# Kernel tuning notes

Measured on AMD Instinct MI355X. Metric: run time of the kernel, lower is better.

## Reference

```python
import jax, jax.numpy as jnp
import numpy as np

D = 256           # input_dim
PROCESS_STEP = 4
N_SUPPORT = 512
BATCH = 32768


def setup_inputs() -> dict:
    key = jax.random.key(0)
    ks = jax.random.split(key, 8)
    H = 2 * D  # LSTMCell hidden size
    scale = 0.05
    return {
        "support_mean": jax.random.normal(ks[0], (N_SUPPORT, D), jnp.float32),
        "support_var": jax.random.uniform(ks[1], (N_SUPPORT, D), jnp.float32),
        "query_mean": jax.random.normal(ks[2], (BATCH, D), jnp.float32),
        "query_var": jax.random.uniform(ks[3], (BATCH, D), jnp.float32),
        # LSTMCell(D, 2D) parameters (PyTorch layout: [4*H, in] / [4*H, H])
        "W_ih": jax.random.normal(ks[4], (4 * H, D), jnp.float32) * scale,
        "W_hh": jax.random.normal(ks[5], (4 * H, H), jnp.float32) * scale,
        "b_ih": jax.random.normal(ks[6], (4 * H,), jnp.float32) * scale,
        "b_hh": jax.random.normal(ks[7], (4 * H,), jnp.float32) * scale,
    }


def _lstm_cell(x, h, c, W_ih, W_hh, b_ih, b_hh):
    # gates: [B, 4H], PyTorch gate order: input, forget, cell(g), output
    gates = x @ W_ih.T + b_ih + h @ W_hh.T + b_hh
    i, f, g, o = jnp.split(gates, 4, axis=1)
    i = jax.nn.sigmoid(i)
    f = jax.nn.sigmoid(f)
    g = jnp.tanh(g)
    o = jax.nn.sigmoid(o)
    c_new = f * c + i * g
    h_new = o * jnp.tanh(c_new)
    return h_new, c_new


def reference(support_mean, support_var, query_mean, query_var,
              W_ih, W_hh, b_ih, b_hh):
    # support_var / query_var are unused by the original forward.
    B = query_mean.shape[0]
    H = 2 * D
    h_r = jnp.zeros((B, H), query_mean.dtype)
    c = jnp.zeros((B, H), query_mean.dtype)
    h = query_mean  # placeholder; overwritten in first step
    for _ in range(PROCESS_STEP):
        h_r_, c = _lstm_cell(query_mean, h_r, c, W_ih, W_hh, b_ih, b_hh)
        h = query_mean + h_r_[:, :D]                       # [B, D]
        attn = jax.nn.softmax(h @ support_mean.T, axis=1)   # [B, S]
        r = attn @ support_mean                              # [B, D]
        h_r = jnp.concatenate((h, r), axis=1)                # [B, 2D]
    matching_scores = jnp.squeeze(h @ support_mean.T)        # [B, S]
    return matching_scores
```

## Files before the change

### kernel.cpp

```cpp
#include <hip/hip_runtime.h>

typedef unsigned int uint;
typedef unsigned short ushort;
typedef __attribute__((ext_vector_type(8))) short bhalf8;
typedef __attribute__((ext_vector_type(4))) float floatx4;

#define D_IN 256
#define NUNIT 256
#define GN 1024
#define NSUP 512
#define BATCH_N 32768
#define LDA_A 768

__device__ __forceinline__ ushort f2b(float f){
  union { float f; uint u; } x; x.f = f;
  uint r = (x.u + 0x7fffu + ((x.u >> 16) & 1u)) >> 16;
  return (ushort)r;
}
__device__ __forceinline__ float b2f(ushort u){
  union { uint u; float f; } x; x.u = ((uint)u) << 16;
  return x.f;
}
__device__ __forceinline__ float sigmf(float x){ return 1.0f / (1.0f + __expf(-x)); }
__device__ __forceinline__ float tanhfast(float x){ return 1.0f - 2.0f / (1.0f + __expf(2.0f * x)); }

__device__ __forceinline__ void stage_rows8(
    ushort* lds_base, const ushort* __restrict__ g, int ld,
    long grow0, int lrow0, int k0, int lane)
{
  const int rsub = lane >> 3;
  const int oct  = (lane & 7) ^ rsub;
  const ushort* gp = g + (grow0 + lrow0 + rsub) * ld + k0 + (oct << 3);
  ushort* lp = lds_base + lrow0 * 64;
  __builtin_amdgcn_global_load_lds(
      (const __attribute__((address_space(1))) void*)gp,
      (__attribute__((address_space(3))) void*)lp, 16, 0, 0);
}

__device__ __forceinline__ void stage_swz4(
    ushort* lds, const ushort* __restrict__ g, int ld, int row0, int k0,
    int wave, int lane)
{
  #pragma unroll
  for (int q = 0; q < 4; q++)
    stage_rows8(lds, g, ld, row0, wave * 32 + q * 8, k0, lane);
}

__device__ __forceinline__ void stage_swz8(
    ushort* lds, const ushort* __restrict__ g, int ld, int row0, int k0,
    int wave, int lane)
{
  #pragma unroll
  for (int q = 0; q < 2; q++)
    stage_rows8(lds, g, ld, row0, wave * 16 + q * 8, k0, lane);
}

__device__ __forceinline__ bhalf8 frag_ld(const ushort* lds, int R, int O, int sx)
{
  return *reinterpret_cast<const bhalf8*>(&lds[R * 64 + (((O ^ sx) & 7) << 3)]);
}

__device__ __forceinline__ bhalf8 frag_ld512(const ushort* lds, int R, int g, int O, int sx)
{
  return *reinterpret_cast<const bhalf8*>(&lds[R * 512 + g * 64 + (((O ^ sx) & 7) << 3)]);
}

__global__ __launch_bounds__(512) void gemm_gq_fused(
    const ushort* __restrict__ Qb,
    const ushort* __restrict__ Wq,
    const float4* __restrict__ biasp,
    uint2* __restrict__ Gq,
    float* __restrict__ cbuf,
    const float* __restrict__ query,
    ushort* __restrict__ Hhi,
    ushort* __restrict__ Hlo)
{
  __shared__ ushort SM[2][8192];

  const int tid  = threadIdx.x;
  const int lane = tid & 63;
  const int wave = tid >> 6;
  const int wrow = (wave >> 1) * 32;
  const int wcol = (wave & 1) * 64;
  const int wg = (blockIdx.x & 7) * (gridDim.x >> 3) + (blockIdx.x >> 3);
  const int bm = wg >> 3;
  const int bn = wg & 7;
  const int rowA0 = bm * 128;
  const int colB0 = bn * 128;

  floatx4 acc[2][4];
  #pragma unroll
  for (int m = 0; m < 2; m++)
    #pragma unroll
    for (int n = 0; n < 4; n++)
      acc[m][n] = (floatx4){0.f, 0.f, 0.f, 0.f};

  const int lr = lane & 15;
  const int lg = lane >> 4;
  const int sx = lane & 7;

  for (int k0 = 0; k0 < 256; k0 += 64) {
    stage_swz8(SM[0], Qb, 256, rowA0, k0, wave, lane);
    stage_swz8(SM[1], Wq, 256, colB0, k0, wave, lane);
    __syncthreads();
    #pragma unroll
    for (int ks = 0; ks < 2; ks++) {
      bhalf8 af[2], bfr[4];
      #pragma unroll
      for (int m = 0; m < 2; m++)
        af[m] = frag_ld(SM[0], wrow + m * 16 + lr, ks * 4 + lg, sx);
      #pragma unroll
      for (int n = 0; n < 4; n++)
        bfr[n] = frag_ld(SM[1], wcol + n * 16 + lr, ks * 4 + lg, sx);
      #pragma unroll
      for (int m = 0; m < 2; m++)
        #pragma unroll
        for (int n = 0; n < 4; n++)
          acc[m][n] = __builtin_amdgcn_mfma_f32_16x16x32_bf16(af[m], bfr[n], acc[m][n], 0, 0, 0);
    }
    __syncthreads();
  }

  ushort* ehi = (ushort*)SM[0];
  ushort* elo = ehi + 128 * 32;
  float*  ec  = (float*)SM[1];

  const int u_loc = (wave & 1) * 16 + lr;
  const int u     = bn * 32 + u_loc;
  const float4 b4 = biasp[u];
  #pragma unroll
  for (int m = 0; m < 2; m++) {
    #pragma unroll
    for (int rr = 0; rr < 4; rr++) {
      const int  rloc = wrow + m * 16 + lg * 4 + rr;
      const long row  = rowA0 + rloc;
      float pi = acc[m][0][rr] + b4.x;
      float pf = acc[m][1][rr] + b4.y;
      float pg = acc[m][2][rr] + b4.z;
      float po = acc[m][3][rr] + b4.w;
      uint2 pk;
      pk.x = (uint)f2b(pi) | ((uint)f2b(pf) << 16);
      pk.y = (uint)f2b(pg) | ((uint)f2b(po) << 16);
      Gq[row * NUNIT + u] = pk;
      float cn = sigmf(pi) * tanhfast(pg);
      ec[rloc * 32 + u_loc] = cn;
      float h = query[row * D_IN + u] + sigmf(po) * tanhfast(cn);
      ushort hh = f2b(h);
      ehi[rloc * 32 + u_loc] = hh;
      elo[rloc * 32 + u_loc] = f2b(h - b2f(hh));
    }
  }
  __syncthreads();
  const int u0 = bn * 32;
  {
    int row = tid >> 2, part = tid & 3;
    *(uint4*)(Hhi + (long)(rowA0 + row) * LDA_A + u0 + part * 8) = ((const uint4*)ehi)[tid];
    *(uint4*)(Hlo + (long)(rowA0 + row) * D_IN + u0 + part * 8) = ((const uint4*)elo)[tid];
  }
  #pragma unroll
  for (int i = tid; i < 1024; i += 512) {
    int row = i >> 3, part = i & 7;
    *(uint4*)(cbuf + (long)(rowA0 + row) * NUNIT + u0 + part * 4) = ((const uint4*)ec)[i];
  }
}

__global__ __launch_bounds__(512) void gemm_gates_fused(
    const ushort* __restrict__ A,
    const ushort* __restrict__ W,
    const uint2* __restrict__ Gq,
    float* __restrict__ cbuf,
    const float* __restrict__ query,
    ushort* __restrict__ Hhi,
    ushort* __restrict__ Hlo)
{
  __shared__ ushort SM[2][2][8192];

  const int tid  = threadIdx.x;
  const int lane = tid & 63;
  const int wave = tid >> 6;
  const int wrow = (wave >> 1) * 32;
  const int wcol = (wave & 1) * 64;
  const int wg = (blockIdx.x & 7) * (gridDim.x >> 3) + (blockIdx.x >> 3);
  const int bm = wg >> 3;
  const int bn = wg & 7;
  const int rowA0 = bm * 128;
  const int colB0 = bn * 128;

  floatx4 acc[2][4];
  #pragma unroll
  for (int m = 0; m < 2; m++)
    #pragma unroll
    for (int n = 0; n < 4; n++)
      acc[m][n] = (floatx4){0.f, 0.f, 0.f, 0.f};

  const int lr = lane & 15;
  const int lg = lane >> 4;
  const int sx = lane & 7;

  stage_swz8(SM[0][0], A, LDA_A, rowA0, 0, wave, lane);
  stage_swz8(SM[0][1], W, 512,   colB0, 0, wave, lane);
  __syncthreads();

  for (int t = 0; t < 8; t++) {
    const int cur = t & 1;
    if (t + 1 < 8) {
      stage_swz8(SM[cur ^ 1][0], A, LDA_A, rowA0, (t + 1) * 64, wave, lane);
      stage_swz8(SM[cur ^ 1][1], W, 512,   colB0, (t + 1) * 64, wave, lane);
    }
    const ushort* As = SM[cur][0];
    const ushort* Bs = SM[cur][1];
    #pragma unroll
    for (int ks = 0; ks < 2; ks++) {
      bhalf8 af[2], bfr[4];
      #pragma unroll
      for (int m = 0; m < 2; m++)
        af[m] = frag_ld(As, wrow + m * 16 + lr, ks * 4 + lg, sx);
      #pragma unroll
      for (int n = 0; n < 4; n++)
        bfr[n] = frag_ld(Bs, wcol + n * 16 + lr, ks * 4 + lg, sx);
      #pragma unroll
      for (int m = 0; m < 2; m++)
        #pragma unroll
        for (int n = 0; n < 4; n++)
          acc[m][n] = __builtin_amdgcn_mfma_f32_16x16x32_bf16(af[m], bfr[n], acc[m][n], 0, 0, 0);
    }
    __syncthreads();
  }

  ushort* ehi = (ushort*)SM[0][0];
  ushort* elo = ehi + 128 * 32;
  float*  ec  = (float*)SM[0][1];

  const int u_loc = (wave & 1) * 16 + lr;
  const int u     = bn * 32 + u_loc;
  #pragma unroll
  for (int m = 0; m < 2; m++) {
    #pragma unroll
    for (int rr = 0; rr < 4; rr++) {
      const int  rloc = wrow + m * 16 + lg * 4 + rr;
      const long row  = rowA0 + rloc;
      uint2 pk = Gq[row * NUNIT + u];
      float pi = acc[m][0][rr] + b2f((ushort)(pk.x & 0xffff));
      float pf = acc[m][1][rr] + b2f((ushort)(pk.x >> 16));
      float pg = acc[m][2][rr] + b2f((ushort)(pk.y & 0xffff));
      float po = acc[m][3][rr] + b2f((ushort)(pk.y >> 16));
      float cn = sigmf(pf) * cbuf[row * NUNIT + u] + sigmf(pi) * tanhfast(pg);
      ec[rloc * 32 + u_loc] = cn;
      float h = query[row * D_IN + u] + sigmf(po) * tanhfast(cn);
      ushort hh = f2b(h);
      ehi[rloc * 32 + u_loc] = hh;
      elo[rloc * 32 + u_loc] = f2b(h - b2f(hh));
    }
  }
  __syncthreads();
  const int u0 = bn * 32;
  {
    int row = tid >> 2, part = tid & 3;
    *(uint4*)(Hhi + (long)(rowA0 + row) * LDA_A + u0 + part * 8) = ((const uint4*)ehi)[tid];
    *(uint4*)(Hlo + (long)(rowA0 + row) * D_IN + u0 + part * 8) = ((const uint4*)elo)[tid];
  }
  #pragma unroll
  for (int i = tid; i < 1024; i += 512) {
    int row = i >> 3, part = i & 7;
    *(uint4*)(cbuf + (long)(rowA0 + row) * NUNIT + u0 + part * 4) = ((const uint4*)ec)[i];
  }
}

__global__ __launch_bounds__(256) void gemm_scores(
    const ushort* __restrict__ Ahi,
    const ushort* __restrict__ Alo,
    const ushort* __restrict__ Bhi, const ushort* __restrict__ Blo,
    float* __restrict__ C)
{
  __shared__ ushort AsH[128 * 64];
  __shared__ ushort AsL[128 * 64];
  __shared__ ushort BsH[128 * 64];
  __shared__ ushort BsL[128 * 64];

  const int tid  = threadIdx.x;
  const int lane = tid & 63;
  const int wave = tid >> 6;
  const int wr = (wave >> 1) * 64;
  const int wc = (wave & 1) * 64;
  const int wg = (blockIdx.x & 7) * (gridDim.x >> 3) + (blockIdx.x >> 3);
  const int bm = wg >> 2;
  const int bn = wg & 3;
  const int rowA0 = bm * 128;
  const int rowB0 = bn * 128;

  floatx4 acc[4][4];
  #pragma unroll
  for (int m = 0; m < 4; m++)
    #pragma unroll
    for (int n = 0; n < 4; n++)
      acc[m][n] = (floatx4){0.f, 0.f, 0.f, 0.f};

  const int lr = lane & 15;
  const int lg = lane >> 4;
  const int sx = lane & 7;

  for (int k0 = 0; k0 < D_IN; k0 += 64) {
    stage_swz4(AsH, Ahi, LDA_A, rowA0, k0, wave, lane);
    stage_swz4(AsL, Alo, D_IN,  rowA0, k0, wave, lane);
    stage_swz4(BsH, Bhi, D_IN,  rowB0, k0, wave, lane);
    stage_swz4(BsL, Blo, D_IN,  rowB0, k0, wave, lane);
    __syncthreads();
    #pragma unroll
    for (int ks = 0; ks < 2; ks++) {
      bhalf8 afh[4], afl[4], bfh[4], bfl[4];
      #pragma unroll
      for (int m = 0; m < 4; m++) {
        afh[m] = frag_ld(AsH, wr + m * 16 + lr, ks * 4 + lg, sx);
        afl[m] = frag_ld(AsL, wr + m * 16 + lr, ks * 4 + lg, sx);
      }
      #pragma unroll
      for (int n = 0; n < 4; n++) {
        bfh[n] = frag_ld(BsH, wc + n * 16 + lr, ks * 4 + lg, sx);
        bfl[n] = frag_ld(BsL, wc + n * 16 + lr, ks * 4 + lg, sx);
      }
      #pragma unroll
      for (int m = 0; m < 4; m++)
        #pragma unroll
        for (int n = 0; n < 4; n++) {
          acc[m][n] = __builtin_amdgcn_mfma_f32_16x16x32_bf16(afl[m], bfh[n], acc[m][n], 0, 0, 0);
          acc[m][n] = __builtin_amdgcn_mfma_f32_16x16x32_bf16(afh[m], bfl[n], acc[m][n], 0, 0, 0);
          acc[m][n] = __builtin_amdgcn_mfma_f32_16x16x32_bf16(afh[m], bfh[n], acc[m][n], 0, 0, 0);
        }
    }
    __syncthreads();
  }

  #pragma unroll
  for (int m = 0; m < 4; m++)
    #pragma unroll
    for (int n = 0; n < 4; n++)
      #pragma unroll
      for (int r = 0; r < 4; r++) {
        int row = rowA0 + wr + m * 16 + lg * 4 + r;
        int col = rowB0 + wc + n * 16 + lr;
        C[(long)row * NSUP + col] = acc[m][n][r];
      }
}

__global__ __launch_bounds__(512) void k_sspv(
    const ushort* __restrict__ Ahi,
    const ushort* __restrict__ Alo,
    const ushort* __restrict__ Shi,
    const ushort* __restrict__ Slo,
    const ushort* __restrict__ STb,
    ushort* __restrict__ Cv)
{
  __shared__ ushort SMEM[65536];
  ushort* Areg = SMEM;
  ushort* Breg = SMEM + 32768;

  const int tid  = threadIdx.x;
  const int lane = tid & 63;
  const int wave = tid >> 6;
  const int wg = (blockIdx.x & 7) * (gridDim.x >> 3) + (blockIdx.x >> 3);
  const long rowA0 = (long)wg * 64;

  const int lr = lane & 15;
  const int lg = lane >> 4;
  const int sx = lane & 7;

  {
    const ushort* asrc = (wave < 4) ? Ahi : Alo;
    const int ald = (wave < 4) ? LDA_A : D_IN;
    ushort* adst = Areg + (wave >> 2) * 16384 + (wave & 3) * 4096;
    const int ak0 = (wave & 3) * 64;
    #pragma unroll
    for (int q = 0; q < 8; q++)
      stage_rows8(adst, asrc, ald, rowA0, q * 8, ak0, lane);
  }
  #pragma unroll
  for (int q = 0; q < 8; q++)
    stage_rows8(Breg, Shi, D_IN, 0, wave * 64 + q * 8, 0, lane);
  __syncthreads();

  floatx4 acc[4][4];
  #pragma unroll
  for (int m = 0; m < 4; m++)
    #pragma unroll
    for (int n = 0; n < 4; n++)
      acc[m][n] = (floatx4){0.f, 0.f, 0.f, 0.f};

  for (int kc = 0; kc < 4; kc++) {
    const ushort* Ah = Areg + kc * 4096;
    const ushort* Al = Areg + 16384 + kc * 4096;
    #pragma unroll
    for (int ks = 0; ks < 2; ks++) {
      bhalf8 afh[4], afl[4], bfh[4];
      #pragma unroll
      for (int m = 0; m < 4; m++) {
        afh[m] = frag_ld(Ah, m * 16 + lr, ks * 4 + lg, sx);
        afl[m] = frag_ld(Al, m * 16 + lr, ks * 4 + lg, sx);
      }
      #pragma unroll
      for (int n = 0; n < 4; n++)
        bfh[n] = frag_ld(Breg, wave * 64 + n * 16 + lr, ks * 4 + lg, sx);
      #pragma unroll
      for (int m = 0; m < 4; m++)
        #pragma unroll
        for (int n = 0; n < 4; n++) {
          acc[m][n] = __builtin_amdgcn_mfma_f32_16x16x32_bf16(afl[m], bfh[n], acc[m][n], 0, 0, 0);
          acc[m][n] = __builtin_amdgcn_mfma_f32_16x16x32_bf16(afh[m], bfh[n], acc[m][n], 0, 0, 0);
        }
    }
    __syncthreads();
    #pragma unroll
    for (int q = 0; q < 8; q++)
      stage_rows8(Breg, Slo, D_IN, 0, wave * 64 + q * 8, kc * 64, lane);
    __syncthreads();
    #pragma unroll
    for (int ks = 0; ks < 2; ks++) {
      bhalf8 afh[4], bfl[4];
      #pragma unroll
      for (int m = 0; m < 4; m++)
        afh[m] = frag_ld(Ah, m * 16 + lr, ks * 4 + lg, sx);
      #pragma unroll
      for (int n = 0; n < 4; n++)
        bfl[n] = frag_ld(Breg, wave * 64 + n * 16 + lr, ks * 4 + lg, sx);
      #pragma unroll
      for (int m = 0; m < 4; m++)
        #pragma unroll
        for (int n = 0; n < 4; n++)
          acc[m][n] = __builtin_amdgcn_mfma_f32_16x16x32_bf16(afh[m], bfl[n], acc[m][n], 0, 0, 0);
    }
    __syncthreads();
    if (kc < 3) {
      #pragma unroll
      for (int q = 0; q < 8; q++)
        stage_rows8(Breg, Shi, D_IN, 0, wave * 64 + q * 8, (kc + 1) * 64, lane);
      __syncthreads();
    }
  }

  float*  scf = (float*)Breg;
  ushort* Ps  = Areg;
  const int po  = (lane >> 1) & 7;
  const int ph4 = (lane & 1) * 4;
  const int pg0 = lane >> 4;

  #pragma unroll
  for (int half = 0; half < 2; half++) {
    #pragma unroll
    for (int mm = 0; mm < 2; mm++) {
      const int m = half * 2 + mm;
      #pragma unroll
      for (int n = 0; n < 4; n++)
        #pragma unroll
        for (int r = 0; r < 4; r++)
          scf[(mm * 16 + lg * 4 + r) * 512 + wave * 64 + n * 16 + lr] = acc[m][n][r];
    }
    __syncthreads();
    #pragma unroll
    for (int j = 0; j < 4; j++) {
      const int rl = wave * 4 + j;
      const int r  = half * 32 + rl;
      const float4* sp = reinterpret_cast<const float4*>(scf + rl * 512);
      float4 v0 = sp[lane];
      float4 v1 = sp[64 + lane];
      float m = fmaxf(fmaxf(fmaxf(v0.x, v0.y), fmaxf(v0.z, v0.w)),
                      fmaxf(fmaxf(v1.x, v1.y), fmaxf(v1.z, v1.w)));
      #pragma unroll
      for (int off = 32; off >= 1; off >>= 1) m = fmaxf(m, __shfl_xor(m, off));
      float e0 = __expf(v0.x - m), e1 = __expf(v0.y - m), e2 = __expf(v0.z - m), e3 = __expf(v0.w - m);
      float e4 = __expf(v1.x - m), e5 = __expf(v1.y - m), e6 = __expf(v1.z - m), e7 = __expf(v1.w - m);
      float s = e0 + e1 + e2 + e3 + e4 + e5 + e6 + e7;
      #pragma unroll
      for (int off = 32; off >= 1; off >>= 1) s += __shfl_xor(s, off);
      float inv = 1.0f / s;
      uint2 p0, p1;
      p0.x = (uint)f2b(e0 * inv) | ((uint)f2b(e1 * inv) << 16);
      p0.y = (uint)f2b(e2 * inv) | ((uint)f2b(e3 * inv) << 16);
      p1.x = (uint)f2b(e4 * inv) | ((uint)f2b(e5 * inv) << 16);
      p1.y = (uint)f2b(e6 * inv) | ((uint)f2b(e7 * inv) << 16);
      const int os = ((po ^ (r & 7)) << 3) + ph4;
      *(uint2*)&Ps[r * 512 + (pg0    ) * 64 + os] = p0;
      *(uint2*)&Ps[r * 512 + (pg0 + 4) * 64 + os] = p1;
    }
    __syncthreads();
  }

  floatx4 pacc[4][2];
  #pragma unroll
  for (int m = 0; m < 4; m++)
    #pragma unroll
    for (int n = 0; n < 2; n++)
      pacc[m][n] = (floatx4){0.f, 0.f, 0.f, 0.f};

  ushort* Bpv = Breg;
  for (int kc = 0; kc < 8; kc++) {
    #pragma unroll
    for (int q = 0; q < 4; q++)
      stage_rows8(Bpv, STb, NSUP, 0, wave * 32 + q * 8, kc * 64, lane);
    __syncthreads();
    #pragma unroll
    for (int ks = 0; ks < 2; ks++) {
      bhalf8 af[4], bfr[2];
      #pragma unroll
      for (int m = 0; m < 4; m++)
        af[m] = frag_ld512(Ps, m * 16 + lr, kc, ks * 4 + lg, sx);
      #pragma unroll
      for (int n = 0; n < 2; n++)
        bfr[n] = frag_ld(Bpv, wave * 32 + n * 16 + lr, ks * 4 + lg, sx);
      #pragma unroll
      for (int m = 0; m < 4; m++)
        #pragma unroll
        for (int n = 0; n < 2; n++)
          pacc[m][n] = __builtin_amdgcn_mfma_f32_16x16x32_bf16(af[m], bfr[n], pacc[m][n], 0, 0, 0);
    }
    __syncthreads();
  }

  ushort* elr = Breg + 16384;
  #pragma unroll
  for (int m = 0; m < 4; m++)
    #pragma unroll
    for (int n = 0; n < 2; n++)
      #pragma unroll
      for (int r = 0; r < 4; r++)
        elr[(m * 16 + lg * 4 + r) * 256 + wave * 32 + n * 16 + lr] = f2b(pacc[m][n][r]);
  __syncthreads();
  #pragma unroll
  for (int i = tid; i < 2048; i += 512) {
    int row = i >> 5, part = i & 31;
    *(uint4*)(Cv + (rowA0 + row) * LDA_A + part * 8) = ((const uint4*)elr)[i];
  }
}

__global__ __launch_bounds__(256) void k_build(
    const float* __restrict__ Wih, const float* __restrict__ Whh,
    const float* __restrict__ bih, const float* __restrict__ bhh,
    const float* __restrict__ S,
    ushort* __restrict__ We, ushort* __restrict__ Wo, ushort* __restrict__ Wq,
    float4* __restrict__ biasp,
    ushort* __restrict__ Shi, ushort* __restrict__ Slo,
    ushort* __restrict__ STb)
{
  int t = blockIdx.x * 256 + threadIdx.x;
  if (t < GN * 512) {
    int c = t >> 9, k = t & 511;
    int unit = (c >> 6) * 16 + (c & 15);
    int gate = (c >> 4) & 3;
    long srow = (long)(gate * 512 + unit);
    We[(long)c * 512 + k] = f2b(Whh[srow * 512 + k]);
    int ko = (k < 256) ? (256 + k) : (k - 256);
    Wo[(long)c * 512 + k] = f2b(Whh[srow * 512 + ko]);
    if (k < 256) Wq[(long)c * 256 + k] = f2b(Wih[srow * 256 + k]);
  }
  if (t < NUNIT) {
    biasp[t] = make_float4(bih[t] + bhh[t],
                           bih[512 + t] + bhh[512 + t],
                           bih[1024 + t] + bhh[1024 + t],
                           bih[1536 + t] + bhh[1536 + t]);
  }
  if (t < NSUP * D_IN) {
    float v = S[t];
    ushort hv = f2b(v);
    Shi[t] = hv;
    Slo[t] = f2b(v - b2f(hv));
    int s = t >> 8, d = t & 255;
    STb[(long)d * NSUP + s] = hv;
  }
}

__global__ __launch_bounds__(256) void k_initq(
    const float* __restrict__ query, ushort* __restrict__ Qb)
{
  long t = (long)blockIdx.x * 256 + threadIdx.x;
  Qb[t] = f2b(query[t]);
}

extern "C" void kernel_launch(void* const* d_in, const int* in_sizes, int n_in,
                              void* d_out, int out_size, void* d_ws, size_t ws_size,
                              hipStream_t stream)
{
  const float* support_mean = (const float*)d_in[0];
  const float* query_mean   = (const float*)d_in[2];
  const float* W_ih = (const float*)d_in[4];
  const float* W_hh = (const float*)d_in[5];
  const float* b_ih = (const float*)d_in[6];
  const float* b_hh = (const float*)d_in[7];
  float* out = (float*)d_out;

  char* ws = (char*)d_ws;
  size_t off = 0;
  auto alloc = [&](size_t bytes) {
    void* p = ws + off;
    off += (bytes + 255) & ~(size_t)255;
    return p;
  };
  ushort* Abuf  = (ushort*)alloc((size_t)BATCH_N * LDA_A * 2);
  ushort* Qb    = (ushort*)alloc((size_t)BATCH_N * D_IN * 2);
  ushort* We    = (ushort*)alloc((size_t)GN * 512 * 2);
  ushort* Wo    = (ushort*)alloc((size_t)GN * 512 * 2);
  ushort* Wq    = (ushort*)alloc((size_t)GN * 256 * 2);
  float4* biasp = (float4*)alloc((size_t)NUNIT * 16);
  ushort* Shi   = (ushort*)alloc((size_t)NSUP * D_IN * 2);
  ushort* Slo   = (ushort*)alloc((size_t)NSUP * D_IN * 2);
  ushort* STb   = (ushort*)alloc((size_t)D_IN * NSUP * 2);
  float*  cbuf  = (float*) alloc((size_t)BATCH_N * NUNIT * 4);
  ushort* Hlo   = (ushort*)alloc((size_t)BATCH_N * D_IN * 2);
  uint2*  Gq    = (uint2*) alloc((size_t)BATCH_N * NUNIT * 8);
  if (off > ws_size) return;

  hipLaunchKernelGGL(k_build, dim3((GN * 512) / 256), dim3(256), 0, stream,
                     W_ih, W_hh, b_ih, b_hh, support_mean,
                     We, Wo, Wq, biasp, Shi, Slo, STb);
  hipLaunchKernelGGL(k_initq, dim3((BATCH_N * D_IN) / 256), dim3(256), 0, stream,
                     query_mean, Qb);

  hipLaunchKernelGGL(gemm_gq_fused,
                     dim3((BATCH_N / 128) * (GN / 128)), dim3(512), 0, stream,
                     Qb, Wq, biasp, Gq, cbuf, query_mean, Abuf + 0, Hlo);

  for (int s = 0; s < 3; s++) {
    const int hoff = (s & 1) * 512;
    hipLaunchKernelGGL(k_sspv, dim3(BATCH_N / 64), dim3(512), 0, stream,
                       Abuf + hoff, Hlo, Shi, Slo, STb, Abuf + 256);
    const int aoff = ((s + 1) == 2) ? 256 : 0;
    const ushort* Wnext = ((s + 1) == 2) ? Wo : We;
    hipLaunchKernelGGL(gemm_gates_fused,
                       dim3((BATCH_N / 128) * (GN / 128)), dim3(512), 0, stream,
                       Abuf + aoff, Wnext, Gq, cbuf, query_mean,
                       Abuf + ((s + 1) & 1) * 512, Hlo);
  }
  hipLaunchKernelGGL(gemm_scores,
                     dim3((BATCH_N / 128) * (NSUP / 128)), dim3(256), 0, stream,
                     Abuf + 512, Hlo, Shi, Slo, out);
}
```

Measured before the change: 469.0 us.

## Halve k_sspv row tile to 32 and shrink LDS to 64KB for occupancy

The attention kernel k_sspv now processes 32 query rows per workgroup instead of 64 and stages the support matrix in 32-wide K chunks with a new 4-way swizzle. LDS use drops from 128KB to 64KB, which could allow two workgroups per CU and doubles the grid size. In exchange, every workgroup still streams the full support matrices, so support-side global traffic and barrier count per row roughly double.

```diff
diff --git a/kernel.cpp b/kernel.cpp
--- a/kernel.cpp
+++ b/kernel.cpp
@@ -37,6 +37,19 @@
       (__attribute__((address_space(3))) void*)lp, 16, 0, 0);
 }
 
+__device__ __forceinline__ void stage_rows16_32(
+    ushort* lds_base, const ushort* __restrict__ g, int ld,
+    long grow0, int lrow0, int k0, int lane)
+{
+  const int rsub = lane >> 2;
+  const int oct  = (lane & 3) ^ ((rsub >> 1) & 3);
+  const ushort* gp = g + (grow0 + lrow0 + rsub) * ld + k0 + (oct << 3);
+  ushort* lp = lds_base + lrow0 * 32;
+  __builtin_amdgcn_global_load_lds(
+      (const __attribute__((address_space(1))) void*)gp,
+      (__attribute__((address_space(3))) void*)lp, 16, 0, 0);
+}
+
 __device__ __forceinline__ void stage_swz4(
     ushort* lds, const ushort* __restrict__ g, int ld, int row0, int k0,
     int wave, int lane)
@@ -58,6 +71,11 @@
 __device__ __forceinline__ bhalf8 frag_ld(const ushort* lds, int R, int O, int sx)
 {
   return *reinterpret_cast<const bhalf8*>(&lds[R * 64 + (((O ^ sx) & 7) << 3)]);
+}
+
+__device__ __forceinline__ bhalf8 frag32_ld(const ushort* lds, int R, int O)
+{
+  return *reinterpret_cast<const bhalf8*>(&lds[R * 32 + (((O ^ (R >> 1)) & 3) << 3)]);
 }
 
 __device__ __forceinline__ bhalf8 frag_ld512(const ushort* lds, int R, int g, int O, int sx)
@@ -350,15 +368,14 @@
     const ushort* __restrict__ STb,
     ushort* __restrict__ Cv)
 {
-  __shared__ ushort SMEM[65536];
-  ushort* Areg = SMEM;
-  ushort* Breg = SMEM + 32768;
+  __shared__ ushort SMEM[32768];
+  ushort* Sbuf = SMEM + 16384;
 
   const int tid  = threadIdx.x;
   const int lane = tid & 63;
   const int wave = tid >> 6;
   const int wg = (blockIdx.x & 7) * (gridDim.x >> 3) + (blockIdx.x >> 3);
-  const long rowA0 = (long)wg * 64;
+  const long rowA0 = (long)wg * 32;
 
   const int lr = lane & 15;
   const int lg = lane >> 4;
@@ -367,77 +384,68 @@
   {
     const ushort* asrc = (wave < 4) ? Ahi : Alo;
     const int ald = (wave < 4) ? LDA_A : D_IN;
-    ushort* adst = Areg + (wave >> 2) * 16384 + (wave & 3) * 4096;
+    ushort* adst = SMEM + (wave >> 2) * 8192 + (wave & 3) * 2048;
     const int ak0 = (wave & 3) * 64;
     #pragma unroll
-    for (int q = 0; q < 8; q++)
+    for (int q = 0; q < 4; q++)
       stage_rows8(adst, asrc, ald, rowA0, q * 8, ak0, lane);
   }
   #pragma unroll
-  for (int q = 0; q < 8; q++)
-    stage_rows8(Breg, Shi, D_IN, 0, wave * 64 + q * 8, 0, lane);
+  for (int q = 0; q < 4; q++)
+    stage_rows16_32(Sbuf, Shi, D_IN, 0, wave * 64 + q * 16, 0, lane);
   __syncthreads();
 
-  floatx4 acc[4][4];
-  #pragma unroll
-  for (int m = 0; m < 4; m++)
+  floatx4 acc[2][4];
+  #pragma unroll
+  for (int m = 0; m < 2; m++)
     #pragma unroll
     for (int n = 0; n < 4; n++)
       acc[m][n] = (floatx4){0.f, 0.f, 0.f, 0.f};
 
-  for (int kc = 0; kc < 4; kc++) {
-    const ushort* Ah = Areg + kc * 4096;
-    const ushort* Al = Areg + 16384 + kc * 4096;
-    #pragma unroll
-    for (int ks = 0; ks < 2; ks++) {
-      bhalf8 afh[4], afl[4], bfh[4];
-      #pragma unroll
-      for (int m = 0; m < 4; m++) {
-        afh[m] = frag_ld(Ah, m * 16 + lr, ks * 4 + lg, sx);
-        afl[m] = frag_ld(Al, m * 16 + lr, ks * 4 + lg, sx);
+  for (int kc = 0; kc < 8; kc++) {
+    const ushort* Ah = SMEM + (kc >> 1) * 2048;
+    const ushort* Al = SMEM + 8192 + (kc >> 1) * 2048;
+    const int O = (kc & 1) * 4 + lg;
+    bhalf8 afh[2], afl[2], bf[4];
+    #pragma unroll
+    for (int m = 0; m < 2; m++) {
+      afh[m] = frag_ld(Ah, m * 16 + lr, O, sx);
+      afl[m] = frag_ld(Al, m * 16 + lr, O, sx);
+    }
+    #pragma unroll
+    for (int n = 0; n < 4; n++)
+      bf[n] = frag32_ld(Sbuf, wave * 64 + n * 16 + lr, lg);
+    #pragma unroll
+    for (int m = 0; m < 2; m++)
+      #pragma unroll
+      for (int n = 0; n < 4; n++) {
+        acc[m][n] = __builtin_amdgcn_mfma_f32_16x16x32_bf16(afl[m], bf[n], acc[m][n], 0, 0, 0);
+        acc[m][n] = __builtin_amdgcn_mfma_f32_16x16x32_bf16(afh[m], bf[n], acc[m][n], 0, 0, 0);
       }
+    __syncthreads();
+    #pragma unroll
+    for (int q = 0; q < 4; q++)
+      stage_rows16_32(Sbuf, Slo, D_IN, 0, wave * 64 + q * 16, kc * 32, lane);
+    __syncthreads();
+    #pragma unroll
+    for (int n = 0; n < 4; n++)
+      bf[n] = frag32_ld(Sbuf, wave * 64 + n * 16 + lr, lg);
+    #pragma unroll
+    for (int m = 0; m < 2; m++)
       #pragma unroll
       for (int n = 0; n < 4; n++)
-        bfh[n] = frag_ld(Breg, wave * 64 + n * 16 + lr, ks * 4 + lg, sx);
-      #pragma unroll
-      for (int m = 0; m < 4; m++)
-        #pragma unroll
-        for (int n = 0; n < 4; n++) {
-          acc[m][n] = __builtin_amdgcn_mfma_f32_16x16x32_bf16(afl[m], bfh[n], acc[m][n], 0, 0, 0);
-          acc[m][n] = __builtin_amdgcn_mfma_f32_16x16x32_bf16(afh[m], bfh[n], acc[m][n], 0, 0, 0);
-        }
-    }
-    __syncthreads();
-    #pragma unroll
-    for (int q = 0; q < 8; q++)
-      stage_rows8(Breg, Slo, D_IN, 0, wave * 64 + q * 8, kc * 64, lane);
-    __syncthreads();
-    #pragma unroll
-    for (int ks = 0; ks < 2; ks++) {
-      bhalf8 afh[4], bfl[4];
-      #pragma unroll
-      for (int m = 0; m < 4; m++)
-        afh[m] = frag_ld(Ah, m * 16 + lr, ks * 4 + lg, sx);
-      #pragma unroll
-      for (int n = 0; n < 4; n++)
-        bfl[n] = frag_ld(Breg, wave * 64 + n * 16 + lr, ks * 4 + lg, sx);
-      #pragma unroll
-      for (int m = 0; m < 4; m++)
-        #pragma unroll
-        for (int n = 0; n < 4; n++)
-          acc[m][n] = __builtin_amdgcn_mfma_f32_16x16x32_bf16(afh[m], bfl[n], acc[m][n], 0, 0, 0);
-    }
-    __syncthreads();
-    if (kc < 3) {
-      #pragma unroll
-      for (int q = 0; q < 8; q++)
-        stage_rows8(Breg, Shi, D_IN, 0, wave * 64 + q * 8, (kc + 1) * 64, lane);
+        acc[m][n] = __builtin_amdgcn_mfma_f32_16x16x32_bf16(afh[m], bf[n], acc[m][n], 0, 0, 0);
+    __syncthreads();
+    if (kc < 7) {
+      #pragma unroll
+      for (int q = 0; q < 4; q++)
+        stage_rows16_32(Sbuf, Shi, D_IN, 0, wave * 64 + q * 16, (kc + 1) * 32, lane);
       __syncthreads();
     }
   }
 
-  float*  scf = (float*)Breg;
-  ushort* Ps  = Areg;
+  float*  scf = (float*)Sbuf;
+  ushort* Ps  = SMEM;
   const int po  = (lane >> 1) & 7;
   const int ph4 = (lane & 1) * 4;
   const int pg0 = lane >> 4;
@@ -445,19 +453,15 @@
   #pragma unroll
   for (int half = 0; half < 2; half++) {
     #pragma unroll
-    for (int mm = 0; mm < 2; mm++) {
-      const int m = half * 2 + mm;
-      #pragma unroll
-      for (int n = 0; n < 4; n++)
-        #pragma unroll
-        for (int r = 0; r < 4; r++)
-          scf[(mm * 16 + lg * 4 + r) * 512 + wave * 64 + n * 16 + lr] = acc[m][n][r];
-    }
-    __syncthreads();
-    #pragma unroll
-    for (int j = 0; j < 4; j++) {
-      const int rl = wave * 4 + j;
-      const int r  = half * 32 + rl;
+    for (int n = 0; n < 4; n++)
+      #pragma unroll
+      for (int r = 0; r < 4; r++)
+        scf[(lg * 4 + r) * 512 + wave * 64 + n * 16 + lr] = acc[half][n][r];
+    __syncthreads();
+    #pragma unroll
+    for (int j = 0; j < 2; j++) {
+      const int rl = wave * 2 + j;
+      const int r  = half * 16 + rl;
       const float4* sp = reinterpret_cast<const float4*>(scf + rl * 512);
       float4 v0 = sp[lane];
       float4 v1 = sp[64 + lane];
@@ -483,14 +487,14 @@
     __syncthreads();
   }
 
-  floatx4 pacc[4][2];
-  #pragma unroll
-  for (int m = 0; m < 4; m++)
+  floatx4 pacc[2][2];
+  #pragma unroll
+  for (int m = 0; m < 2; m++)
     #pragma unroll
     for (int n = 0; n < 2; n++)
       pacc[m][n] = (floatx4){0.f, 0.f, 0.f, 0.f};
 
-  ushort* Bpv = Breg;
+  ushort* Bpv = SMEM + 16384;
   for (int kc = 0; kc < 8; kc++) {
     #pragma unroll
     for (int q = 0; q < 4; q++)
@@ -498,15 +502,15 @@
     __syncthreads();
     #pragma unroll
     for (int ks = 0; ks < 2; ks++) {
-      bhalf8 af[4], bfr[2];
-      #pragma unroll
-      for (int m = 0; m < 4; m++)
+      bhalf8 af[2], bfr[2];
+      #pragma unroll
+      for (int m = 0; m < 2; m++)
         af[m] = frag_ld512(Ps, m * 16 + lr, kc, ks * 4 + lg, sx);
       #pragma unroll
       for (int n = 0; n < 2; n++)
         bfr[n] = frag_ld(Bpv, wave * 32 + n * 16 + lr, ks * 4 + lg, sx);
       #pragma unroll
-      for (int m = 0; m < 4; m++)
+      for (int m = 0; m < 2; m++)
         #pragma unroll
         for (int n = 0; n < 2; n++)
           pacc[m][n] = __builtin_amdgcn_mfma_f32_16x16x32_bf16(af[m], bfr[n], pacc[m][n], 0, 0, 0);
@@ -514,9 +518,9 @@
     __syncthreads();
   }
 
-  ushort* elr = Breg + 16384;
-  #pragma unroll
-  for (int m = 0; m < 4; m++)
+  ushort* elr = SMEM + 16384;
+  #pragma unroll
+  for (int m = 0; m < 2; m++)
     #pragma unroll
     for (int n = 0; n < 2; n++)
       #pragma unroll
@@ -524,7 +528,7 @@
         elr[(m * 16 + lg * 4 + r) * 256 + wave * 32 + n * 16 + lr] = f2b(pacc[m][n][r]);
   __syncthreads();
   #pragma unroll
-  for (int i = tid; i < 2048; i += 512) {
+  for (int i = tid; i < 1024; i += 512) {
     int row = i >> 5, part = i & 31;
     *(uint4*)(Cv + (rowA0 + row) * LDA_A + part * 8) = ((const uint4*)elr)[i];
   }
@@ -618,7 +622,7 @@
 
   for (int s = 0; s < 3; s++) {
     const int hoff = (s & 1) * 512;
-    hipLaunchKernelGGL(k_sspv, dim3(BATCH_N / 64), dim3(512), 0, stream,
+    hipLaunchKernelGGL(k_sspv, dim3(BATCH_N / 32), dim3(512), 0, stream,
                        Abuf + hoff, Hlo, Shi, Slo, STb, Abuf + 256);
     const int aoff = ((s + 1) == 2) ? 256 : 0;
     const ushort* Wnext = ((s + 1) == 2) ? Wo : We;
```

Result: slower. 482.1 us (+2.8%).
